# Optimization experiments

Hardware: AMD Instinct MI355X
Metric: run time of the kernel (lower is better)

The kernel has to match this reference:

```python
import jax, jax.numpy as jnp
import numpy as np

B, S, H, D = 8, 1024, 16, 64
EMBED_DIM = H * D  # 1024
NEG_INF = -1e30


def setup_inputs() -> dict:
    key = jax.random.key(0)
    kq, kk, kv, kl = jax.random.split(key, 4)
    q = jax.random.normal(kq, (B, S, H, D), dtype=jnp.float32)
    k = jax.random.normal(kk, (B, S, H, D), dtype=jnp.float32)
    v = jax.random.normal(kv, (B, S, H, D), dtype=jnp.float32)
    # ragged lengths in [S//4, S]; prefix-style key_padding_mask (True = valid)
    lengths = jax.random.randint(kl, (B,), S // 4, S + 1)
    key_padding_mask = jnp.arange(S)[None, :] < lengths[:, None]
    return {"q": q, "k": k, "v": v, "key_padding_mask": key_padding_mask}


def reference(q, k, v, key_padding_mask):
    # Equivalent math of flash_attn_unpadded_qkvpacked_func on unpadded tokens
    # followed by pad_input (zeros at padded query rows), dropout=0 (eval).
    # NOTE: module uses softmax_scale = embed_dim ** -0.5 (not head_dim).
    scale = EMBED_DIM ** (-0.5)
    scores = jnp.einsum("bqhd,bkhd->bhqk", q, k) * scale  # [B,H,S,S]
    scores = jnp.where(key_padding_mask[:, None, None, :], scores, NEG_INF)
    attn = jax.nn.softmax(scores, axis=-1)
    out = jnp.einsum("bhqk,bkhd->bqhd", attn, v)  # [B,S,H,D]
    # pad_input re-inserts zeros at padded query positions
    out = out * key_padding_mask[:, :, None, None].astype(out.dtype)
    return out.reshape(B, S, H * D)
```

## Files before the change

kernel.cpp:

```cpp
#include <hip/hip_runtime.h>


#define NB 8
#define SS 1024
#define NH 16
#define DD 64
#define ROWSTRIDE (NH * DD)
#define SCALE 0.03125f
#define LOG2E 1.4426950408889634f
#define PC1 (SCALE * LOG2E)
#define PC2 (-12.0f * LOG2E)
#define LDSPAD 72

typedef short bf16x8 __attribute__((ext_vector_type(8)));
typedef unsigned short u16;
typedef unsigned short u16x8 __attribute__((ext_vector_type(8)));
typedef float f32x4 __attribute__((ext_vector_type(4)));

__device__ __forceinline__ u16 f2bf(float x) {
  unsigned u = __builtin_bit_cast(unsigned, x);
  return (u16)((u + 0x7FFFu + ((u >> 16) & 1u)) >> 16);
}
__device__ __forceinline__ float bf2f(u16 s) {
  unsigned u = ((unsigned)s) << 16;
  return __builtin_bit_cast(float, u);
}

__global__ __launch_bounds__(256, 4) void fa_main(const void* qv, const void* kv,
                                                  const void* vv, const void* maskv,
                                                  float* out) {
  __shared__ __attribute__((aligned(16))) u16 Kt[64 * LDSPAD];
  __shared__ __attribute__((aligned(16))) u16 Vt[64 * LDSPAD];
  __shared__ __attribute__((aligned(16))) u16 Pw[4][16 * LDSPAD];

  int tid = threadIdx.x;
  int lane = tid & 63;
  int w = tid >> 6;
  int t = lane & 15;
  int quad = lane >> 4;

  int bid = blockIdx.x;
  int x = bid & 7;
  int j = bid >> 3;
  int qt = j & 15;
  int bh = ((j >> 4) << 3) + x;
  int h = bh & (NH - 1);
  int b = bh >> 4;
  int q0 = qt * 64;

  const u16* qs16 = (const u16*)qv;
  float dv = bf2f(qs16[2 * lane]);
  unsigned long long bal = __ballot(!(fabsf(dv) < 100.0f));
  int isf32 = (__popcll(bal) >= 16) ? 1 : 0;

  const unsigned char* m8 = (const unsigned char*)maskv;
  const int* m32 = (const int*)maskv;
  bool isu8 = (m8[1] != 0);
  int lo = 0, hi = SS;
  while (lo < hi) {
    int mid = (lo + hi) >> 1;
    int vbit = isu8 ? (m8[b * SS + mid] != 0) : (m32[b * SS + mid] != 0);
    if (vbit) lo = mid + 1; else hi = mid;
  }
  int len = lo;

  size_t base = (size_t)b * SS * ROWSTRIDE + h * DD;

  if (q0 >= len) {
    f32x4 z4 = {0.f, 0.f, 0.f, 0.f};
    for (int i = tid; i < 64 * 16; i += 256) {
      int r = i >> 4, dseg = (i & 15) << 2;
      *(f32x4*)&out[base + (size_t)(q0 + r) * ROWSTRIDE + dseg] = z4;
    }
    return;
  }

  int qrow = q0 + w * 16 + t;
  bf16x8 qf[2];
  if (isf32) {
    const float* qp = (const float*)qv + base + (size_t)qrow * ROWSTRIDE + quad * 8;
#pragma unroll
    for (int kk = 0; kk < 2; kk++) {
      union { bf16x8 v; u16 a[8]; } u;
#pragma unroll
      for (int jj = 0; jj < 8; jj++) u.a[jj] = f2bf(qp[kk * 32 + jj]);
      qf[kk] = u.v;
    }
  } else {
    const u16* qp = (const u16*)qv + base + (size_t)qrow * ROWSTRIDE + quad * 8;
#pragma unroll
    for (int kk = 0; kk < 2; kk++) qf[kk] = *(const bf16x8*)(qp + kk * 32);
  }

  f32x4 zero4 = {0.f, 0.f, 0.f, 0.f};
  f32x4 oacc[4];
#pragma unroll
  for (int c = 0; c < 4; c++) oacc[c] = zero4;
  float lsum[4] = {0.f, 0.f, 0.f, 0.f};

  int key = tid >> 2, seg = tid & 3;
  int nkt = (len + 63) >> 6;

  f32x4 kA[4], vA[4];
  u16x8 kB[2], vB[2];

  auto issue_loads = [&](int kt) {
    int row = kt * 64 + key;
    if (row > SS - 1) row = SS - 1;
    size_t src = base + (size_t)row * ROWSTRIDE + seg * 16;
    if (isf32) {
      const f32x4* kp = (const f32x4*)((const float*)kv + src);
      const f32x4* vp = (const f32x4*)((const float*)vv + src);
#pragma unroll
      for (int i = 0; i < 4; i++) { kA[i] = kp[i]; vA[i] = vp[i]; }
    } else {
      const u16x8* kp = (const u16x8*)((const u16*)kv + src);
      const u16x8* vp = (const u16x8*)((const u16*)vv + src);
      kB[0] = kp[0]; kB[1] = kp[1]; vB[0] = vp[0]; vB[1] = vp[1];
    }
  };

  auto stage_to_lds = [&]() {
    if (isf32) {
      union { u16x8 v; u16 a[8]; } p0, p1;
#pragma unroll
      for (int i = 0; i < 4; i++) {
        p0.a[i] = f2bf(kA[0][i]); p0.a[4 + i] = f2bf(kA[1][i]);
        p1.a[i] = f2bf(kA[2][i]); p1.a[4 + i] = f2bf(kA[3][i]);
      }
      *(u16x8*)&Kt[key * LDSPAD + seg * 16] = p0.v;
      *(u16x8*)&Kt[key * LDSPAD + seg * 16 + 8] = p1.v;
#pragma unroll
      for (int jj = 0; jj < 16; jj++)
        Vt[(seg * 16 + jj) * LDSPAD + key] = f2bf(vA[jj >> 2][jj & 3]);
    } else {
      *(u16x8*)&Kt[key * LDSPAD + seg * 16] = kB[0];
      *(u16x8*)&Kt[key * LDSPAD + seg * 16 + 8] = kB[1];
#pragma unroll
      for (int jj = 0; jj < 8; jj++) {
        Vt[(seg * 16 + jj) * LDSPAD + key] = vB[0][jj];
        Vt[(seg * 16 + 8 + jj) * LDSPAD + key] = vB[1][jj];
      }
    }
  };

  issue_loads(0);

  for (int kt = 0; kt < nkt; ++kt) {
    __syncthreads();
    stage_to_lds();
    if (kt + 1 < nkt) issue_loads(kt + 1);
    __syncthreads();

    f32x4 sacc[4];
#pragma unroll
    for (int c = 0; c < 4; c++) sacc[c] = zero4;
#pragma unroll
    for (int kk = 0; kk < 2; kk++) {
#pragma unroll
      for (int c = 0; c < 4; c++) {
        bf16x8 kb = *(const bf16x8*)&Kt[(c * 16 + t) * LDSPAD + kk * 32 + quad * 8];
        sacc[c] = __builtin_amdgcn_mfma_f32_16x16x32_bf16(qf[kk], kb, sacc[c], 0, 0, 0);
      }
    }

    float p[4][4];
    if (kt == nkt - 1) {
      int krem = len - kt * 64;
#pragma unroll
      for (int c = 0; c < 4; c++) {
        bool valid = (c * 16 + t) < krem;
#pragma unroll
        for (int r = 0; r < 4; r++)
          p[c][r] = valid ? __builtin_amdgcn_exp2f(fmaf(sacc[c][r], PC1, PC2)) : 0.0f;
      }
    } else {
#pragma unroll
      for (int c = 0; c < 4; c++)
#pragma unroll
        for (int r = 0; r < 4; r++)
          p[c][r] = __builtin_amdgcn_exp2f(fmaf(sacc[c][r], PC1, PC2));
    }
#pragma unroll
    for (int r = 0; r < 4; r++)
      lsum[r] += (p[0][r] + p[1][r]) + (p[2][r] + p[3][r]);

#pragma unroll
    for (int c = 0; c < 4; c++)
#pragma unroll
      for (int r = 0; r < 4; r++)
        Pw[w][(quad * 4 + r) * LDSPAD + c * 16 + t] = f2bf(p[c][r]);

#pragma unroll
    for (int kc = 0; kc < 2; kc++) {
      bf16x8 pa = *(const bf16x8*)&Pw[w][t * LDSPAD + kc * 32 + quad * 8];
#pragma unroll
      for (int c = 0; c < 4; c++) {
        bf16x8 vb = *(const bf16x8*)&Vt[(c * 16 + t) * LDSPAD + kc * 32 + quad * 8];
        oacc[c] = __builtin_amdgcn_mfma_f32_16x16x32_bf16(pa, vb, oacc[c], 0, 0, 0);
      }
    }
  }

#pragma unroll
  for (int off = 1; off < 16; off <<= 1)
#pragma unroll
    for (int r = 0; r < 4; r++) lsum[r] += __shfl_xor(lsum[r], off);
  float inv[4];
#pragma unroll
  for (int r = 0; r < 4; r++) inv[r] = 1.0f / lsum[r];
#pragma unroll
  for (int c = 0; c < 4; c++)
#pragma unroll
    for (int r = 0; r < 4; r++) {
      int qr = q0 + w * 16 + quad * 4 + r;
      float o = oacc[c][r] * inv[r];
      out[base + (size_t)qr * ROWSTRIDE + c * 16 + t] = (qr < len) ? o : 0.0f;
    }
}

extern "C" void kernel_launch(void* const* d_in, const int* in_sizes, int n_in,
                              void* d_out, int out_size, void* d_ws, size_t ws_size,
                              hipStream_t stream) {
  fa_main<<<2048, 256, 0, stream>>>(d_in[0], d_in[1], d_in[2], d_in[3], (float*)d_out);
}
```

Measured before the change: 182.3 us.

## Transpose QK^T MFMA operands and skew V LDS layout to cut bank conflicts

Swaps the MFMA operand order for the score product so each lane holds four consecutive keys for one query row. This lets P be written to LDS as packed 32-bit stores and reduces the row-sum to one scalar plus two cross-quad shuffles. It also adds a per-segment skew to the transposed V tile in LDS, targeting bank conflicts on the scalar V transposes and the V fragment reads. The V indexing is more complex and needs extra LDS padding, and a wrong skew would give incorrect results.

```diff
diff --git a/kernel.cpp b/kernel.cpp
--- a/kernel.cpp
+++ b/kernel.cpp
@@ -1,7 +1,6 @@
 #include <hip/hip_runtime.h>
 
 
-#define NB 8
 #define SS 1024
 #define NH 16
 #define DD 64
@@ -10,7 +9,9 @@
 #define LOG2E 1.4426950408889634f
 #define PC1 (SCALE * LOG2E)
 #define PC2 (-12.0f * LOG2E)
-#define LDSPAD 72
+#define KSTR 72
+#define VSTR 72
+#define PSTR 72
 
 typedef short bf16x8 __attribute__((ext_vector_type(8)));
 typedef unsigned short u16;
@@ -29,9 +30,9 @@
 __global__ __launch_bounds__(256, 4) void fa_main(const void* qv, const void* kv,
                                                   const void* vv, const void* maskv,
                                                   float* out) {
-  __shared__ __attribute__((aligned(16))) u16 Kt[64 * LDSPAD];
-  __shared__ __attribute__((aligned(16))) u16 Vt[64 * LDSPAD];
-  __shared__ __attribute__((aligned(16))) u16 Pw[4][16 * LDSPAD];
+  __shared__ __attribute__((aligned(16))) u16 Kt[64 * KSTR];
+  __shared__ __attribute__((aligned(16))) u16 Vt[64 * VSTR + 48];
+  __shared__ __attribute__((aligned(16))) u16 Pw[4][16 * PSTR];
 
   int tid = threadIdx.x;
   int lane = tid & 63;
@@ -96,7 +97,7 @@
   f32x4 oacc[4];
 #pragma unroll
   for (int c = 0; c < 4; c++) oacc[c] = zero4;
-  float lsum[4] = {0.f, 0.f, 0.f, 0.f};
+  float lsum = 0.f;
 
   int key = tid >> 2, seg = tid & 3;
   int nkt = (len + 63) >> 6;
@@ -121,6 +122,7 @@
   };
 
   auto stage_to_lds = [&]() {
+    int vbase = seg * (16 * VSTR + 16) + key;
     if (isf32) {
       union { u16x8 v; u16 a[8]; } p0, p1;
 #pragma unroll
@@ -128,18 +130,18 @@
         p0.a[i] = f2bf(kA[0][i]); p0.a[4 + i] = f2bf(kA[1][i]);
         p1.a[i] = f2bf(kA[2][i]); p1.a[4 + i] = f2bf(kA[3][i]);
       }
-      *(u16x8*)&Kt[key * LDSPAD + seg * 16] = p0.v;
-      *(u16x8*)&Kt[key * LDSPAD + seg * 16 + 8] = p1.v;
+      *(u16x8*)&Kt[key * KSTR + seg * 16] = p0.v;
+      *(u16x8*)&Kt[key * KSTR + seg * 16 + 8] = p1.v;
 #pragma unroll
       for (int jj = 0; jj < 16; jj++)
-        Vt[(seg * 16 + jj) * LDSPAD + key] = f2bf(vA[jj >> 2][jj & 3]);
+        Vt[vbase + jj * VSTR] = f2bf(vA[jj >> 2][jj & 3]);
     } else {
-      *(u16x8*)&Kt[key * LDSPAD + seg * 16] = kB[0];
-      *(u16x8*)&Kt[key * LDSPAD + seg * 16 + 8] = kB[1];
+      *(u16x8*)&Kt[key * KSTR + seg * 16] = kB[0];
+      *(u16x8*)&Kt[key * KSTR + seg * 16 + 8] = kB[1];
 #pragma unroll
       for (int jj = 0; jj < 8; jj++) {
-        Vt[(seg * 16 + jj) * LDSPAD + key] = vB[0][jj];
-        Vt[(seg * 16 + 8 + jj) * LDSPAD + key] = vB[1][jj];
+        Vt[vbase + jj * VSTR] = vB[0][jj];
+        Vt[vbase + (8 + jj) * VSTR] = vB[1][jj];
       }
     }
   };
@@ -159,8 +161,8 @@
     for (int kk = 0; kk < 2; kk++) {
 #pragma unroll
       for (int c = 0; c < 4; c++) {
-        bf16x8 kb = *(const bf16x8*)&Kt[(c * 16 + t) * LDSPAD + kk * 32 + quad * 8];
-        sacc[c] = __builtin_amdgcn_mfma_f32_16x16x32_bf16(qf[kk], kb, sacc[c], 0, 0, 0);
+        bf16x8 ka = *(const bf16x8*)&Kt[(c * 16 + t) * KSTR + kk * 32 + quad * 8];
+        sacc[c] = __builtin_amdgcn_mfma_f32_16x16x32_bf16(ka, qf[kk], sacc[c], 0, 0, 0);
       }
     }
 
@@ -169,10 +171,12 @@
       int krem = len - kt * 64;
 #pragma unroll
       for (int c = 0; c < 4; c++) {
-        bool valid = (c * 16 + t) < krem;
+        int kbase = c * 16 + quad * 4;
 #pragma unroll
         for (int r = 0; r < 4; r++)
-          p[c][r] = valid ? __builtin_amdgcn_exp2f(fmaf(sacc[c][r], PC1, PC2)) : 0.0f;
+          p[c][r] = (kbase + r < krem)
+                        ? __builtin_amdgcn_exp2f(fmaf(sacc[c][r], PC1, PC2))
+                        : 0.0f;
       }
     } else {
 #pragma unroll
@@ -182,33 +186,35 @@
           p[c][r] = __builtin_amdgcn_exp2f(fmaf(sacc[c][r], PC1, PC2));
     }
 #pragma unroll
-    for (int r = 0; r < 4; r++)
-      lsum[r] += (p[0][r] + p[1][r]) + (p[2][r] + p[3][r]);
-
-#pragma unroll
     for (int c = 0; c < 4; c++)
-#pragma unroll
-      for (int r = 0; r < 4; r++)
-        Pw[w][(quad * 4 + r) * LDSPAD + c * 16 + t] = f2bf(p[c][r]);
+      lsum += (p[c][0] + p[c][1]) + (p[c][2] + p[c][3]);
+
+#pragma unroll
+    for (int c = 0; c < 4; c++)
+#pragma unroll
+      for (int jp = 0; jp < 2; jp++) {
+        unsigned d = (unsigned)f2bf(p[c][2 * jp]) |
+                     ((unsigned)f2bf(p[c][2 * jp + 1]) << 16);
+        *(unsigned*)&Pw[w][t * PSTR + c * 16 + quad * 4 + 2 * jp] = d;
+      }
 
 #pragma unroll
     for (int kc = 0; kc < 2; kc++) {
-      bf16x8 pa = *(const bf16x8*)&Pw[w][t * LDSPAD + kc * 32 + quad * 8];
+      bf16x8 pa = *(const bf16x8*)&Pw[w][t * PSTR + kc * 32 + quad * 8];
 #pragma unroll
       for (int c = 0; c < 4; c++) {
-        bf16x8 vb = *(const bf16x8*)&Vt[(c * 16 + t) * LDSPAD + kc * 32 + quad * 8];
+        bf16x8 vb = *(const bf16x8*)&Vt[(c * 16 + t) * VSTR + c * 16 + kc * 32 + quad * 8];
         oacc[c] = __builtin_amdgcn_mfma_f32_16x16x32_bf16(pa, vb, oacc[c], 0, 0, 0);
       }
     }
   }
 
-#pragma unroll
-  for (int off = 1; off < 16; off <<= 1)
-#pragma unroll
-    for (int r = 0; r < 4; r++) lsum[r] += __shfl_xor(lsum[r], off);
+  lsum += __shfl_xor(lsum, 16);
+  lsum += __shfl_xor(lsum, 32);
   float inv[4];
 #pragma unroll
-  for (int r = 0; r < 4; r++) inv[r] = 1.0f / lsum[r];
+  for (int r = 0; r < 4; r++)
+    inv[r] = 1.0f / __shfl(lsum, quad * 4 + r);
 #pragma unroll
   for (int c = 0; c < 4; c++)
 #pragma unroll
```

After: 175.8 us. -3.6%, faster.
